# Performance work log

Measured on AMD Instinct MI355X. Metric: run time of the kernel, lower is better.

The kernel has to match this reference:

```python
import jax, jax.numpy as jnp
import numpy as np

HIDDEN = 512

def setup_inputs() -> dict:
    key = jax.random.key(0)
    k1, k2, k3, k4 = jax.random.split(key, 4)
    B, T, H = 64, 4096, HIDDEN
    hidden = jax.random.normal(k1, (B, H), dtype=jnp.float32)
    encoder_outputs = jax.random.normal(k2, (B, T, H), dtype=jnp.float32)
    # nn.Linear(H, H) parameters: weight [H, H], bias [H]
    lim = 1.0 / np.sqrt(H)
    W = jax.random.uniform(k3, (H, H), minval=-lim, maxval=lim, dtype=jnp.float32)
    b = jax.random.uniform(k4, (H,), minval=-lim, maxval=lim, dtype=jnp.float32)
    return {"hidden": hidden, "encoder_outputs": encoder_outputs, "W": W, "b": b}

def reference(hidden, encoder_outputs, W, b):
    # method == 'general': energy[b,t] = dot(Linear(encoder_outputs[b,t]), hidden[b])
    # projected: [B, T, H] = enc @ W.T + b
    proj = jnp.einsum('bth,oh->bto', encoder_outputs, W) + b
    scores = jnp.einsum('bth,bh->bt', proj, hidden)  # [B, T]
    attn = jax.nn.softmax(scores, axis=1)            # row softmax over time
    return attn[:, None, :]                           # [B, 1, T]
```

## Files before the change

kernel.cpp:

```cpp
#include <hip/hip_runtime.h>
#include <hip/hip_bf16.h>
#include <math.h>

#define HID 512
#define TLEN 4096
#define BATCH 64

__global__ __launch_bounds__(HID) void proj_kernel(const float* __restrict__ hidden,
                                                   const float* __restrict__ W,
                                                   float* __restrict__ v) {
    __shared__ float hs[HID];
    const int b = blockIdx.x;
    const int h = threadIdx.x;
    hs[h] = hidden[b * HID + h];
    __syncthreads();
    float s = 0.f;
#pragma unroll 16
    for (int o = 0; o < HID; ++o) {
        s = fmaf(hs[o], W[o * HID + h], s);
    }
    v[b * HID + h] = s;
}

__global__ __launch_bounds__(256) void score_kernel(const float* __restrict__ enc,
                                                    const float* __restrict__ v,
                                                    float* __restrict__ scores) {
    const int b    = blockIdx.y;
    const int wave = threadIdx.x >> 6;
    const int lane = threadIdx.x & 63;
    const int t0   = blockIdx.x * 64 + wave * 16;

    const float4* v4 = (const float4*)(v + b * HID);
    const float4  va = v4[lane];
    const float4  vb = v4[64 + lane];

    const float4* e4 = (const float4*)(enc + (size_t)b * TLEN * HID);

#pragma unroll 4
    for (int i = 0; i < 16; ++i) {
        const int t = t0 + i;
        const float4* row = e4 + (size_t)t * (HID / 4);
        const float4 ea = row[lane];
        const float4 eb = row[64 + lane];
        float s = ea.x * va.x + ea.y * va.y + ea.z * va.z + ea.w * va.w
                + eb.x * vb.x + eb.y * vb.y + eb.z * vb.z + eb.w * vb.w;
#pragma unroll
        for (int off = 32; off; off >>= 1) s += __shfl_xor(s, off, 64);
        if (lane == 0) scores[b * TLEN + t] = s;
    }
}

__global__ __launch_bounds__(1024) void softmax_kernel(const float* __restrict__ scores,
                                                       float* __restrict__ out) {
    __shared__ float redm[16];
    __shared__ float reds[16];
    const int b    = blockIdx.x;
    const int tid  = threadIdx.x;
    const int wave = tid >> 6;
    const int lane = tid & 63;

    const float4 x = ((const float4*)(scores + b * TLEN))[tid];

    float m = fmaxf(fmaxf(x.x, x.y), fmaxf(x.z, x.w));
#pragma unroll
    for (int off = 32; off; off >>= 1) m = fmaxf(m, __shfl_xor(m, off, 64));
    if (lane == 0) redm[wave] = m;
    __syncthreads();
    if (wave == 0) {
        float t = (lane < 16) ? redm[lane] : -INFINITY;
#pragma unroll
        for (int off = 8; off; off >>= 1) t = fmaxf(t, __shfl_xor(t, off, 64));
        if (lane == 0) redm[0] = t;
    }
    __syncthreads();
    m = redm[0];

    float4 e;
    e.x = __expf(x.x - m);
    e.y = __expf(x.y - m);
    e.z = __expf(x.z - m);
    e.w = __expf(x.w - m);
    float sum = e.x + e.y + e.z + e.w;
#pragma unroll
    for (int off = 32; off; off >>= 1) sum += __shfl_xor(sum, off, 64);
    if (lane == 0) reds[wave] = sum;
    __syncthreads();
    if (wave == 0) {
        float t = (lane < 16) ? reds[lane] : 0.f;
#pragma unroll
        for (int off = 8; off; off >>= 1) t += __shfl_xor(t, off, 64);
        if (lane == 0) reds[0] = t;
    }
    __syncthreads();
    const float inv = 1.0f / reds[0];

    float4 o4;
    o4.x = e.x * inv; o4.y = e.y * inv; o4.z = e.z * inv; o4.w = e.w * inv;
    ((float4*)(out + b * TLEN))[tid] = o4;
}

extern "C" void kernel_launch(void* const* d_in, const int* in_sizes, int n_in,
                              void* d_out, int out_size, void* d_ws, size_t ws_size,
                              hipStream_t stream) {
    const float* hidden = (const float*)d_in[0];
    const float* enc    = (const float*)d_in[1];
    const float* W      = (const float*)d_in[2];
    float* out = (float*)d_out;

    float* v      = (float*)d_ws;
    float* scores = v + BATCH * HID;

    proj_kernel<<<dim3(BATCH), dim3(HID), 0, stream>>>(hidden, W, v);
    score_kernel<<<dim3(TLEN / 64, BATCH), dim3(256), 0, stream>>>(enc, v, scores);
    softmax_kernel<<<dim3(BATCH), dim3(1024), 0, stream>>>(scores, out);
}
```

Before: 699.2 us.

## Process eight rows per wave with 8-lane groups and stage v in LDS

The score kernel now splits each wave into eight groups of eight lanes, so every group reduces a different encoder row and each lane loads 16 float4s per row. v is staged in shared memory instead of registers, and each block covers 128 rows instead of 64. The intent is more memory loads in flight per wave and a cheaper shuffle reduction (3 steps instead of 6). In exchange, each lane's accesses within a row are strided, with 128-byte contiguous segments per group, and the inner loop adds LDS reads.

```diff
diff --git a/kernel.cpp b/kernel.cpp
--- a/kernel.cpp
+++ b/kernel.cpp
@@ -1,5 +1,4 @@
 #include <hip/hip_runtime.h>
-#include <hip/hip_bf16.h>
 #include <math.h>
 
 #define HID 512
@@ -25,28 +24,39 @@
 __global__ __launch_bounds__(256) void score_kernel(const float* __restrict__ enc,
                                                     const float* __restrict__ v,
                                                     float* __restrict__ scores) {
+    __shared__ float4 vs[HID / 4];
     const int b    = blockIdx.y;
-    const int wave = threadIdx.x >> 6;
-    const int lane = threadIdx.x & 63;
-    const int t0   = blockIdx.x * 64 + wave * 16;
+    const int tid  = threadIdx.x;
+    const int wave = tid >> 6;
+    const int lane = tid & 63;
+    const int g    = lane >> 3;
+    const int j    = lane & 7;
 
-    const float4* v4 = (const float4*)(v + b * HID);
-    const float4  va = v4[lane];
-    const float4  vb = v4[64 + lane];
+    if (tid < HID / 4) vs[tid] = ((const float4*)(v + b * HID))[tid];
+    __syncthreads();
 
     const float4* e4 = (const float4*)(enc + (size_t)b * TLEN * HID);
+    const int rowBase = blockIdx.x * 128 + wave * 32;
 
-#pragma unroll 4
-    for (int i = 0; i < 16; ++i) {
-        const int t = t0 + i;
+#pragma unroll
+    for (int batch = 0; batch < 4; ++batch) {
+        const int t = rowBase + batch * 8 + g;
         const float4* row = e4 + (size_t)t * (HID / 4);
-        const float4 ea = row[lane];
-        const float4 eb = row[64 + lane];
-        float s = ea.x * va.x + ea.y * va.y + ea.z * va.z + ea.w * va.w
-                + eb.x * vb.x + eb.y * vb.y + eb.z * vb.z + eb.w * vb.w;
+        float s0 = 0.f, s1 = 0.f;
 #pragma unroll
-        for (int off = 32; off; off >>= 1) s += __shfl_xor(s, off, 64);
-        if (lane == 0) scores[b * TLEN + t] = s;
+        for (int k = 0; k < 16; k += 2) {
+            const float4 a0 = row[k * 8 + j];
+            const float4 a1 = row[(k + 1) * 8 + j];
+            const float4 v0 = vs[k * 8 + j];
+            const float4 v1 = vs[(k + 1) * 8 + j];
+            s0 += a0.x * v0.x + a0.y * v0.y + a0.z * v0.z + a0.w * v0.w;
+            s1 += a1.x * v1.x + a1.y * v1.y + a1.z * v1.z + a1.w * v1.w;
+        }
+        float s = s0 + s1;
+        s += __shfl_xor(s, 1, 64);
+        s += __shfl_xor(s, 2, 64);
+        s += __shfl_xor(s, 4, 64);
+        if (j == 0) scores[b * TLEN + t] = s;
     }
 }
 
@@ -111,6 +121,6 @@
     float* scores = v + BATCH * HID;
 
     proj_kernel<<<dim3(BATCH), dim3(HID), 0, stream>>>(hidden, W, v);
-    score_kernel<<<dim3(TLEN / 64, BATCH), dim3(256), 0, stream>>>(enc, v, scores);
+    score_kernel<<<dim3(TLEN / 128, BATCH), dim3(256), 0, stream>>>(enc, v, scores);
     softmax_kernel<<<dim3(BATCH), dim3(1024), 0, stream>>>(scores, out);
 }
```

Result: no change. 702.8 us (+0.5%).
